# Kernel tuning notes

Hardware: AMD Instinct MI355X
Metric: run time of the kernel (lower is better)

## Reference

```python
import jax, jax.numpy as jnp
import numpy as np

N = 50000      # nodes
E = 800000     # edges (avg degree 16)
D = 64         # node feature dim
DE = 32        # edge feature dim
H = 256        # MLP hidden dim


def setup_inputs() -> dict:
    key = jax.random.key(0)
    k0, k1, k2, k3, k4 = jax.random.split(key, 5)
    x = jax.random.normal(k0, (N, D), dtype=jnp.float32)
    edge_index = jax.random.randint(k1, (2, E), 0, N)
    edge_attr = jax.random.normal(k2, (E, DE), dtype=jnp.float32)
    fan_in1 = 2 * D + DE  # 160
    W1 = jax.random.normal(k3, (fan_in1, H), dtype=jnp.float32) / np.float32(np.sqrt(fan_in1))
    b1 = jnp.zeros((H,), dtype=jnp.float32)
    W2 = jax.random.normal(k4, (H, D), dtype=jnp.float32) / np.float32(np.sqrt(H))
    b2 = jnp.zeros((D,), dtype=jnp.float32)
    return {"x": x, "edge_index": edge_index, "edge_attr": edge_attr,
            "W1": W1, "b1": b1, "W2": W2, "b2": b2}


def reference(x, edge_index, edge_attr, W1, b1, W2, b2):
    row, col = edge_index[0], edge_index[1]
    # gather endpoint features + edge features -> [E, 2D+DE]
    feats = jnp.concatenate([x[row], x[col], edge_attr], axis=-1)
    # MLP: Linear -> ReLU -> Linear
    h = jax.nn.relu(feats @ W1 + b1)          # [E, H]
    out = h @ W2 + b2                          # [E, D]
    # scatter-max aggregate by source node (row), dim_size = N
    agg = jax.ops.segment_max(out, row, num_segments=N)  # [N, D]
    # PyG's old scatter_('max') zero-fills empty slots
    agg = jnp.where(jnp.isneginf(agg), jnp.float32(0.0), agg)
    return (agg, out)
```

## Files before the change

### kernel.cpp

```cpp
#include <hip/hip_runtime.h>
#include <hip/hip_bf16.h>
#include <math.h>

#define NNODES 50000
#define NEDGES 800000
#define CHUNKS (NEDGES / 32)
#define NBLK 256
#define GWAVES (NBLK * 16)

using short8 = __attribute__((ext_vector_type(8))) short;
using f32x4  = __attribute__((ext_vector_type(4))) float;
using f32x16 = __attribute__((ext_vector_type(16))) float;
using u32x4  = __attribute__((ext_vector_type(4))) unsigned;

__device__ __forceinline__ short f2b(float v) {
    return __builtin_bit_cast(short, __float2bfloat16(v));
}
__device__ __forceinline__ unsigned cvt2(float a, float b) {
    return (unsigned)(unsigned short)f2b(a) | ((unsigned)(unsigned short)f2b(b) << 16);
}

__global__ void prep_all(const float* __restrict__ x, short* __restrict__ xb,
                         const float* __restrict__ W1, const float* __restrict__ W2,
                         short* __restrict__ wpk, const int* __restrict__ ei,
                         unsigned* __restrict__ cnt)
{
    int b = blockIdx.x;
    if (b < 3125) {
        int i = b * 256 + threadIdx.x;
        float4 v = reinterpret_cast<const float4*>(x)[i];
        short4 o;
        o.x = f2b(v.x); o.y = f2b(v.y); o.z = f2b(v.z); o.w = f2b(v.w);
        reinterpret_cast<short4*>(xb)[i] = o;
    } else if (b < 6250) {
        int e = (b - 3125) * 256 + threadIdx.x;
        atomicAdd(&cnt[ei[e]], 1u);
    } else {
        int i = (b - 6250) * 256 + threadIdx.x;
        if (i < 40960) {
            int k = i >> 8, n = i & 255;
            int lane = (n & 31) + (((k >> 3) & 1) << 5);
            wpk[(((n >> 5) * 10 + (k >> 4)) * 64 + lane) * 8 + (k & 7)] = f2b(W1[i]);
        }
        if (i < 16384) {
            int k = i >> 6, n = i & 63;
            int lane = (n & 31) + (((k >> 3) & 1) << 5);
            wpk[40960 + (((n >> 5) * 16 + (k >> 4)) * 64 + lane) * 8 + (k & 7)] = f2b(W2[i]);
        }
    }
}

__global__ __launch_bounds__(1024)
void csr_scan1(const unsigned* __restrict__ cnt, unsigned* __restrict__ offs,
               unsigned* __restrict__ bsum) {
    __shared__ unsigned sbuf[1024];
    int t = threadIdx.x, i = blockIdx.x * 1024 + t;
    unsigned v = (i < NNODES) ? cnt[i] : 0u;
    sbuf[t] = v;
    __syncthreads();
    for (int off = 1; off < 1024; off <<= 1) {
        unsigned add = (t >= off) ? sbuf[t - off] : 0u;
        __syncthreads();
        sbuf[t] += add;
        __syncthreads();
    }
    if (i < NNODES) offs[i] = sbuf[t];
    if (t == 1023) bsum[blockIdx.x] = sbuf[1023];
}

__global__ void csr_scan2(unsigned* __restrict__ bsum) {
    int t = threadIdx.x;
    unsigned v = (t < 49) ? bsum[t] : 0u;
    unsigned orig = v;
    for (int off = 1; off < 64; off <<= 1) {
        unsigned n = __shfl_up(v, off, 64);
        if (t >= off) v += n;
    }
    if (t < 49) bsum[t] = v - orig;
}

__global__ __launch_bounds__(1024)
void csr_scan3(const unsigned* __restrict__ cnt, unsigned* __restrict__ offs,
               const unsigned* __restrict__ bsum) {
    int i = blockIdx.x * 1024 + threadIdx.x;
    if (i < NNODES)       offs[i] = offs[i] - cnt[i] + bsum[blockIdx.x];
    else if (i == NNODES) offs[i] = NEDGES;
}

__global__ void csr_place(const int* __restrict__ ei, const unsigned* __restrict__ offs,
                          unsigned* __restrict__ cur, unsigned* __restrict__ elist,
                          unsigned* __restrict__ pos) {
    int e = blockIdx.x * 256 + threadIdx.x;
    if (e < NEDGES) {
        int r = ei[e];
        unsigned p = offs[r] + atomicAdd(&cur[r], 1u);
        elist[p] = (unsigned)e;
        if (pos) pos[e] = p;
    }
}

template<bool STORECSR>
__global__ __launch_bounds__(1024, 4)
void edgeconv_main(const short* __restrict__ xb, const int* __restrict__ ei,
                   const float* __restrict__ ea, const short* __restrict__ wpk,
                   const float* __restrict__ b1, const float* __restrict__ b2,
                   const unsigned* __restrict__ pos,
                   float* __restrict__ outbuf, unsigned* __restrict__ outcsr)
{
    __shared__ short wlds[57344];

    for (int i = threadIdx.x; i < 7168; i += 1024)
        reinterpret_cast<short8*>(wlds)[i] = reinterpret_cast<const short8*>(wpk)[i];
    __syncthreads();

    const short* w1s = wlds;
    const short* w2s = wlds + 40960;
    const int lane = threadIdx.x & 63;
    const int wave = threadIdx.x >> 6;
    const int l32 = lane & 31, hi = lane >> 5;
    const int gw = blockIdx.x * 16 + wave;

    int r = 0, cc = 0; unsigned pv = 0;
    if (gw < CHUNKS) {
        int e0 = gw * 32 + l32;
        r  = ei[e0];
        cc = ei[NEDGES + e0];
        if (STORECSR) pv = pos[e0];
    }

    for (int c = gw; c < CHUNKS; c += GWAVES) {
        const int e = c * 32 + l32;

        int cn = c + GWAVES;
        int r_n = 0, cc_n = 0; unsigned pv_n = 0;
        if (cn < CHUNKS) {
            int e1 = cn * 32 + l32;
            r_n  = ei[e1];
            cc_n = ei[NEDGES + e1];
            if (STORECSR) pv_n = pos[e1];
        }

        short8 fx[10];
        #pragma unroll
        for (int ks = 0; ks < 4; ++ks)
            fx[ks] = *reinterpret_cast<const short8*>(xb + r * 64 + ks * 16 + hi * 8);
        #pragma unroll
        for (int ks = 0; ks < 4; ++ks)
            fx[4 + ks] = *reinterpret_cast<const short8*>(xb + cc * 64 + ks * 16 + hi * 8);
        #pragma unroll
        for (int ks = 0; ks < 2; ++ks) {
            const float4* p = reinterpret_cast<const float4*>(ea + (size_t)e * 32 + ks * 16 + hi * 8);
            float4 a = p[0], b = p[1];
            u32x4 uu;
            uu[0] = cvt2(a.x, a.y); uu[1] = cvt2(a.z, a.w);
            uu[2] = cvt2(b.x, b.y); uu[3] = cvt2(b.z, b.w);
            fx[8 + ks] = __builtin_bit_cast(short8, uu);
        }

        f32x16 acc2[2];
        #pragma unroll
        for (int t2 = 0; t2 < 2; ++t2)
            #pragma unroll
            for (int g = 0; g < 4; ++g) {
                float4 bb = *reinterpret_cast<const float4*>(b2 + t2 * 32 + g * 8 + hi * 4);
                acc2[t2][g * 4 + 0] = bb.x; acc2[t2][g * 4 + 1] = bb.y;
                acc2[t2][g * 4 + 2] = bb.z; acc2[t2][g * 4 + 3] = bb.w;
            }

        #pragma unroll 1
        for (int t = 0; t < 8; ++t) {
            f32x16 acc1;
            #pragma unroll
            for (int g = 0; g < 4; ++g) {
                float4 bb = *reinterpret_cast<const float4*>(b1 + t * 32 + g * 8 + hi * 4);
                acc1[g * 4 + 0] = bb.x; acc1[g * 4 + 1] = bb.y;
                acc1[g * 4 + 2] = bb.z; acc1[g * 4 + 3] = bb.w;
            }
            #pragma unroll
            for (int ks = 0; ks < 10; ++ks) {
                short8 wf = *reinterpret_cast<const short8*>(
                    w1s + ((t * 10 + ks) * 64 + lane) * 8);
                acc1 = __builtin_amdgcn_mfma_f32_32x32x16_bf16(wf, fx[ks], acc1, 0, 0, 0);
            }
            #pragma unroll
            for (int ksl = 0; ksl < 2; ++ksl) {
                int q0 = ksl * 8;
                unsigned D0 = cvt2(fmaxf(acc1[q0 + 0], 0.f), fmaxf(acc1[q0 + 1], 0.f));
                unsigned D1 = cvt2(fmaxf(acc1[q0 + 2], 0.f), fmaxf(acc1[q0 + 3], 0.f));
                unsigned D2 = cvt2(fmaxf(acc1[q0 + 4], 0.f), fmaxf(acc1[q0 + 5], 0.f));
                unsigned D3 = cvt2(fmaxf(acc1[q0 + 6], 0.f), fmaxf(acc1[q0 + 7], 0.f));
                asm volatile("v_permlane32_swap_b32 %0, %1" : "+v"(D0), "+v"(D2));
                asm volatile("v_permlane32_swap_b32 %0, %1" : "+v"(D1), "+v"(D3));
                u32x4 bu; bu[0] = D0; bu[1] = D1; bu[2] = D2; bu[3] = D3;
                short8 hb = __builtin_bit_cast(short8, bu);

                int ks2 = t * 2 + ksl;
                short8 w20 = *reinterpret_cast<const short8*>(w2s + (ks2 * 64 + lane) * 8);
                short8 w21 = *reinterpret_cast<const short8*>(w2s + ((16 + ks2) * 64 + lane) * 8);
                acc2[0] = __builtin_amdgcn_mfma_f32_32x32x16_bf16(w20, hb, acc2[0], 0, 0, 0);
                acc2[1] = __builtin_amdgcn_mfma_f32_32x32x16_bf16(w21, hb, acc2[1], 0, 0, 0);
            }
        }

        #pragma unroll
        for (int t2 = 0; t2 < 2; ++t2)
            #pragma unroll
            for (int g = 0; g < 4; ++g) {
                f32x4 v;
                v[0] = acc2[t2][g * 4 + 0]; v[1] = acc2[t2][g * 4 + 1];
                v[2] = acc2[t2][g * 4 + 2]; v[3] = acc2[t2][g * 4 + 3];
                *reinterpret_cast<f32x4*>(outbuf + (size_t)e * 64 + t2 * 32 + g * 8 + hi * 4) = v;
                if (STORECSR) {
                    uint2 pk;
                    pk.x = cvt2(v[0], v[1]);
                    pk.y = cvt2(v[2], v[3]);
                    *reinterpret_cast<uint2*>(outcsr + (size_t)pv * 32 + t2 * 16 + g * 4 + hi * 2) = pk;
                }
            }

        r = r_n; cc = cc_n; pv = pv_n;
    }
}

__global__ __launch_bounds__(256)
void agg_csr(const unsigned* __restrict__ offs, const unsigned* __restrict__ outcsr,
             float* __restrict__ agg)
{
    const int wave = threadIdx.x >> 6, lane = threadIdx.x & 63;
    const int l32 = lane & 31, half = lane >> 5;
    const int node = blockIdx.x * 4 + wave;
    if (node >= NNODES) return;
    const unsigned s = offs[node], eend = offs[node + 1];
    float m0 = -INFINITY, m1 = -INFINITY;
    for (unsigned p = s + half; p < eend; p += 2) {
        unsigned u = outcsr[(size_t)p * 32 + l32];
        m0 = fmaxf(m0, __builtin_bit_cast(float, u << 16));
        m1 = fmaxf(m1, __builtin_bit_cast(float, u & 0xFFFF0000u));
    }
    m0 = fmaxf(m0, __shfl_xor(m0, 32, 64));
    m1 = fmaxf(m1, __shfl_xor(m1, 32, 64));
    if (half == 0) {
        float2 o;
        o.x = (s == eend) ? 0.0f : m0;
        o.y = (s == eend) ? 0.0f : m1;
        *reinterpret_cast<float2*>(agg + (size_t)node * 64 + l32 * 2) = o;
    }
}

__global__ __launch_bounds__(256)
void agg_list(const unsigned* __restrict__ offs, const unsigned* __restrict__ elist,
              const float* __restrict__ outbuf, float* __restrict__ agg)
{
    const int wave = threadIdx.x >> 6, lane = threadIdx.x & 63;
    const int node = blockIdx.x * 4 + wave;
    if (node >= NNODES) return;
    const unsigned s = offs[node], eend = offs[node + 1];
    float m0 = -INFINITY, m1 = -INFINITY, m2 = -INFINITY, m3 = -INFINITY;
    unsigned p = s;
    for (; p + 4 <= eend; p += 4) {
        float a = __builtin_nontemporal_load(outbuf + (size_t)elist[p + 0] * 64 + lane);
        float b = __builtin_nontemporal_load(outbuf + (size_t)elist[p + 1] * 64 + lane);
        float c = __builtin_nontemporal_load(outbuf + (size_t)elist[p + 2] * 64 + lane);
        float d = __builtin_nontemporal_load(outbuf + (size_t)elist[p + 3] * 64 + lane);
        m0 = fmaxf(m0, a); m1 = fmaxf(m1, b);
        m2 = fmaxf(m2, c); m3 = fmaxf(m3, d);
    }
    for (; p < eend; ++p)
        m0 = fmaxf(m0, __builtin_nontemporal_load(outbuf + (size_t)elist[p] * 64 + lane));
    float m = fmaxf(fmaxf(m0, m1), fmaxf(m2, m3));
    agg[(size_t)node * 64 + lane] = (s == eend) ? 0.0f : m;
}

extern "C" void kernel_launch(void* const* d_in, const int* in_sizes, int n_in,
                              void* d_out, int out_size, void* d_ws, size_t ws_size,
                              hipStream_t stream)
{
    const float* x  = (const float*)d_in[0];
    const int*   ei = (const int*)d_in[1];
    const float* ea = (const float*)d_in[2];
    const float* W1 = (const float*)d_in[3];
    const float* b1 = (const float*)d_in[4];
    const float* W2 = (const float*)d_in[5];
    const float* b2 = (const float*)d_in[6];

    float* aggp = (float*)d_out;
    float* outp = aggp + (size_t)NNODES * 64;

    short*    xb   = (short*)d_ws;
    short*    wpk  = (short*)((char*)d_ws + 6400000);
    unsigned* meta = (unsigned*)((char*)d_ws + 6514688);
    unsigned* cnt   = meta;
    unsigned* cur   = meta + 50000;
    unsigned* offs  = meta + 100000;
    unsigned* bsum  = meta + 150016;
    unsigned* elist = meta + 150144;
    unsigned* pos   = meta + 950144;
    unsigned* outcsr = meta + 1750144;

    const size_t NEED = 6514688ULL + 1750144ULL * 4ULL + 102400000ULL;
    const bool big = ws_size >= NEED;

    (void)hipMemsetAsync(cnt, 0, 100000 * sizeof(unsigned), stream);
    prep_all<<<6410, 256, 0, stream>>>(x, xb, W1, W2, wpk, ei, cnt);
    csr_scan1<<<49, 1024, 0, stream>>>(cnt, offs, bsum);
    csr_scan2<<<1, 64, 0, stream>>>(bsum);
    csr_scan3<<<49, 1024, 0, stream>>>(cnt, offs, bsum);
    csr_place<<<NEDGES / 256, 256, 0, stream>>>(ei, offs, cur, elist,
                                                big ? pos : (unsigned*)nullptr);
    if (big) {
        edgeconv_main<true><<<NBLK, 1024, 0, stream>>>(xb, ei, ea, wpk, b1, b2,
                                                       pos, outp, outcsr);
        agg_csr<<<(NNODES + 3) / 4, 256, 0, stream>>>(offs, outcsr, aggp);
    } else {
        edgeconv_main<false><<<NBLK, 1024, 0, stream>>>(xb, ei, ea, wpk, b1, b2,
                                                        nullptr, outp, nullptr);
        agg_list<<<(NNODES + 3) / 4, 256, 0, stream>>>(offs, elist, outp, aggp);
    }
}
```

Measured before the change: 355.6 us.

## Store bf16 edge outputs in edge order and gather via elist in aggregation

The edge kernel now writes the bf16 copy of each edge output at the edge's own index instead of scattering it to its CSR slot, so the pos array and its per-edge load are no longer needed. The aggregation kernel instead gathers through elist, reading scattered 128-byte rows. The change also splits the first-layer MFMA chain into two independent accumulators to shorten the dependency chain, makes the fp32 output stores nontemporal, and drops the occupancy hint from the launch bounds. The trade is coalesced writes and less bookkeeping in exchange for an extra indirection and random reads during aggregation.

```diff
diff --git a/kernel.cpp b/kernel.cpp
--- a/kernel.cpp
+++ b/kernel.cpp
@@ -88,24 +88,21 @@
 }
 
 __global__ void csr_place(const int* __restrict__ ei, const unsigned* __restrict__ offs,
-                          unsigned* __restrict__ cur, unsigned* __restrict__ elist,
-                          unsigned* __restrict__ pos) {
+                          unsigned* __restrict__ cur, unsigned* __restrict__ elist) {
     int e = blockIdx.x * 256 + threadIdx.x;
     if (e < NEDGES) {
         int r = ei[e];
         unsigned p = offs[r] + atomicAdd(&cur[r], 1u);
         elist[p] = (unsigned)e;
-        if (pos) pos[e] = p;
-    }
-}
-
-template<bool STORECSR>
-__global__ __launch_bounds__(1024, 4)
+    }
+}
+
+template<bool STOREB16>
+__global__ __launch_bounds__(1024)
 void edgeconv_main(const short* __restrict__ xb, const int* __restrict__ ei,
                    const float* __restrict__ ea, const short* __restrict__ wpk,
                    const float* __restrict__ b1, const float* __restrict__ b2,
-                   const unsigned* __restrict__ pos,
-                   float* __restrict__ outbuf, unsigned* __restrict__ outcsr)
+                   float* __restrict__ outbuf, unsigned* __restrict__ ob16)
 {
     __shared__ short wlds[57344];
 
@@ -120,24 +117,22 @@
     const int l32 = lane & 31, hi = lane >> 5;
     const int gw = blockIdx.x * 16 + wave;
 
-    int r = 0, cc = 0; unsigned pv = 0;
+    int r = 0, cc = 0;
     if (gw < CHUNKS) {
         int e0 = gw * 32 + l32;
         r  = ei[e0];
         cc = ei[NEDGES + e0];
-        if (STORECSR) pv = pos[e0];
     }
 
     for (int c = gw; c < CHUNKS; c += GWAVES) {
         const int e = c * 32 + l32;
 
         int cn = c + GWAVES;
-        int r_n = 0, cc_n = 0; unsigned pv_n = 0;
+        int r_n = 0, cc_n = 0;
         if (cn < CHUNKS) {
             int e1 = cn * 32 + l32;
             r_n  = ei[e1];
             cc_n = ei[NEDGES + e1];
-            if (STORECSR) pv_n = pos[e1];
         }
 
         short8 fx[10];
@@ -169,19 +164,26 @@
 
         #pragma unroll 1
         for (int t = 0; t < 8; ++t) {
-            f32x16 acc1;
+            f32x16 acc1, acc1b;
             #pragma unroll
             for (int g = 0; g < 4; ++g) {
                 float4 bb = *reinterpret_cast<const float4*>(b1 + t * 32 + g * 8 + hi * 4);
                 acc1[g * 4 + 0] = bb.x; acc1[g * 4 + 1] = bb.y;
                 acc1[g * 4 + 2] = bb.z; acc1[g * 4 + 3] = bb.w;
-            }
-            #pragma unroll
-            for (int ks = 0; ks < 10; ++ks) {
-                short8 wf = *reinterpret_cast<const short8*>(
+                acc1b[g * 4 + 0] = 0.f; acc1b[g * 4 + 1] = 0.f;
+                acc1b[g * 4 + 2] = 0.f; acc1b[g * 4 + 3] = 0.f;
+            }
+            #pragma unroll
+            for (int ks = 0; ks < 10; ks += 2) {
+                short8 wfa = *reinterpret_cast<const short8*>(
                     w1s + ((t * 10 + ks) * 64 + lane) * 8);
-                acc1 = __builtin_amdgcn_mfma_f32_32x32x16_bf16(wf, fx[ks], acc1, 0, 0, 0);
-            }
+                short8 wfb = *reinterpret_cast<const short8*>(
+                    w1s + ((t * 10 + ks + 1) * 64 + lane) * 8);
+                acc1  = __builtin_amdgcn_mfma_f32_32x32x16_bf16(wfa, fx[ks],     acc1,  0, 0, 0);
+                acc1b = __builtin_amdgcn_mfma_f32_32x32x16_bf16(wfb, fx[ks + 1], acc1b, 0, 0, 0);
+            }
+            acc1 = acc1 + acc1b;
+
             #pragma unroll
             for (int ksl = 0; ksl < 2; ++ksl) {
                 int q0 = ksl * 8;
@@ -209,22 +211,23 @@
                 f32x4 v;
                 v[0] = acc2[t2][g * 4 + 0]; v[1] = acc2[t2][g * 4 + 1];
                 v[2] = acc2[t2][g * 4 + 2]; v[3] = acc2[t2][g * 4 + 3];
-                *reinterpret_cast<f32x4*>(outbuf + (size_t)e * 64 + t2 * 32 + g * 8 + hi * 4) = v;
-                if (STORECSR) {
+                __builtin_nontemporal_store(v,
+                    reinterpret_cast<f32x4*>(outbuf + (size_t)e * 64 + t2 * 32 + g * 8 + hi * 4));
+                if (STOREB16) {
                     uint2 pk;
                     pk.x = cvt2(v[0], v[1]);
                     pk.y = cvt2(v[2], v[3]);
-                    *reinterpret_cast<uint2*>(outcsr + (size_t)pv * 32 + t2 * 16 + g * 4 + hi * 2) = pk;
+                    *reinterpret_cast<uint2*>(ob16 + (size_t)e * 32 + t2 * 16 + g * 4 + hi * 2) = pk;
                 }
             }
 
-        r = r_n; cc = cc_n; pv = pv_n;
+        r = r_n; cc = cc_n;
     }
 }
 
 __global__ __launch_bounds__(256)
-void agg_csr(const unsigned* __restrict__ offs, const unsigned* __restrict__ outcsr,
-             float* __restrict__ agg)
+void agg_b16(const unsigned* __restrict__ offs, const unsigned* __restrict__ elist,
+             const unsigned* __restrict__ ob16, float* __restrict__ agg)
 {
     const int wave = threadIdx.x >> 6, lane = threadIdx.x & 63;
     const int l32 = lane & 31, half = lane >> 5;
@@ -233,7 +236,8 @@
     const unsigned s = offs[node], eend = offs[node + 1];
     float m0 = -INFINITY, m1 = -INFINITY;
     for (unsigned p = s + half; p < eend; p += 2) {
-        unsigned u = outcsr[(size_t)p * 32 + l32];
+        unsigned e = elist[p];
+        unsigned u = ob16[(size_t)e * 32 + l32];
         m0 = fmaxf(m0, __builtin_bit_cast(float, u << 16));
         m1 = fmaxf(m1, __builtin_bit_cast(float, u & 0xFFFF0000u));
     }
@@ -258,15 +262,14 @@
     float m0 = -INFINITY, m1 = -INFINITY, m2 = -INFINITY, m3 = -INFINITY;
     unsigned p = s;
     for (; p + 4 <= eend; p += 4) {
-        float a = __builtin_nontemporal_load(outbuf + (size_t)elist[p + 0] * 64 + lane);
-        float b = __builtin_nontemporal_load(outbuf + (size_t)elist[p + 1] * 64 + lane);
-        float c = __builtin_nontemporal_load(outbuf + (size_t)elist[p + 2] * 64 + lane);
-        float d = __builtin_nontemporal_load(outbuf + (size_t)elist[p + 3] * 64 + lane);
+        float a = outbuf[(size_t)elist[p + 0] * 64 + lane];
+        float b = outbuf[(size_t)elist[p + 1] * 64 + lane];
+        float c = outbuf[(size_t)elist[p + 2] * 64 + lane];
+        float d = outbuf[(size_t)elist[p + 3] * 64 + lane];
         m0 = fmaxf(m0, a); m1 = fmaxf(m1, b);
         m2 = fmaxf(m2, c); m3 = fmaxf(m3, d);
     }
-    for (; p < eend; ++p)
-        m0 = fmaxf(m0, __builtin_nontemporal_load(outbuf + (size_t)elist[p] * 64 + lane));
+    for (; p < eend; ++p) m0 = fmaxf(m0, outbuf[(size_t)elist[p] * 64 + lane]);
     float m = fmaxf(fmaxf(m0, m1), fmaxf(m2, m3));
     agg[(size_t)node * 64 + lane] = (s == eend) ? 0.0f : m;
 }
@@ -294,10 +297,9 @@
     unsigned* offs  = meta + 100000;
     unsigned* bsum  = meta + 150016;
     unsigned* elist = meta + 150144;
-    unsigned* pos   = meta + 950144;
-    unsigned* outcsr = meta + 1750144;
-
-    const size_t NEED = 6514688ULL + 1750144ULL * 4ULL + 102400000ULL;
+    unsigned* ob16  = meta + 950144;
+
+    const size_t NEED = 6514688ULL + 950144ULL * 4ULL + 102400000ULL;
     const bool big = ws_size >= NEED;
 
     (void)hipMemsetAsync(cnt, 0, 100000 * sizeof(unsigned), stream);
@@ -305,15 +307,14 @@
     csr_scan1<<<49, 1024, 0, stream>>>(cnt, offs, bsum);
     csr_scan2<<<1, 64, 0, stream>>>(bsum);
     csr_scan3<<<49, 1024, 0, stream>>>(cnt, offs, bsum);
-    csr_place<<<NEDGES / 256, 256, 0, stream>>>(ei, offs, cur, elist,
-                                                big ? pos : (unsigned*)nullptr);
+    csr_place<<<NEDGES / 256, 256, 0, stream>>>(ei, offs, cur, elist);
     if (big) {
         edgeconv_main<true><<<NBLK, 1024, 0, stream>>>(xb, ei, ea, wpk, b1, b2,
-                                                       pos, outp, outcsr);
-        agg_csr<<<(NNODES + 3) / 4, 256, 0, stream>>>(offs, outcsr, aggp);
+                                                       outp, ob16);
+        agg_b16<<<(NNODES + 3) / 4, 256, 0, stream>>>(offs, elist, ob16, aggp);
     } else {
         edgeconv_main<false><<<NBLK, 1024, 0, stream>>>(xb, ei, ea, wpk, b1, b2,
-                                                        nullptr, outp, nullptr);
+                                                        outp, nullptr);
         agg_list<<<(NNODES + 3) / 4, 256, 0, stream>>>(offs, elist, outp, aggp);
     }
 }
```

Result: slower. 398.9 us (+12.2%).
